# Performance work log

Hardware: AMD Instinct MI355X
Metric: run time of the kernel (lower is better)

Reference implementation:

```python
import jax, jax.numpy as jnp
import numpy as np

NEG_SLOPE = 0.2

def gat_conv(x, src, dst, W, a_src, a_dst, bias, N):
    # PyG GATConv, heads=1: h = xW; e_ij = LeakyReLU(a_src.h_j + a_dst.h_i)
    h = x @ W                                   # [N, H]
    as_ = h @ a_src                             # [N]
    ad_ = h @ a_dst                             # [N]
    e = jax.nn.leaky_relu(as_[src] + ad_[dst], NEG_SLOPE)   # [E]
    m = jax.ops.segment_max(e, dst, num_segments=N)          # per-target max
    w = jnp.exp(e - m[dst])
    denom = jax.ops.segment_sum(w, dst, num_segments=N)
    alpha = w / (denom[dst] + 1e-16)                          # [E]
    out = jax.ops.segment_sum(alpha[:, None] * h[src], dst, num_segments=N)
    return out + bias


def setup_inputs() -> dict:
    key = jax.random.key(0)
    N, E, D, H, A = 20000, 320000, 256, 256, 8
    ks = jax.random.split(key, 16)
    s = lambda k, shp, fan: jax.random.normal(k, shp, jnp.float32) * (1.0 / np.sqrt(fan))
    return {
        "obs": jax.random.normal(ks[0], (N, D), jnp.float32),
        "edge_index": jax.random.randint(ks[1], (2, E), 0, N, dtype=jnp.int32),
        "W1": s(ks[2], (D, H), D), "a1_src": s(ks[3], (H,), H), "a1_dst": s(ks[4], (H,), H), "b1": jnp.zeros((H,), jnp.float32),
        "W2": s(ks[5], (H, H), H), "a2_src": s(ks[6], (H,), H), "a2_dst": s(ks[7], (H,), H), "b2": jnp.zeros((H,), jnp.float32),
        "Wm1": s(ks[8], (H, H), H), "bm1": jnp.zeros((H,), jnp.float32),
        "Wm2": s(ks[9], (H, A), H), "bm2": jnp.zeros((A,), jnp.float32),
    }


def reference(obs, edge_index, W1, a1_src, a1_dst, b1, W2, a2_src, a2_dst, b2, Wm1, bm1, Wm2, bm2):
    N = obs.shape[0]
    loops = jnp.arange(N, dtype=edge_index.dtype)
    src = jnp.concatenate([edge_index[0], loops])   # add self-loops (PyG default)
    dst = jnp.concatenate([edge_index[1], loops])
    x = jax.nn.relu(gat_conv(obs, src, dst, W1, a1_src, a1_dst, b1, N))
    x = jax.nn.relu(gat_conv(x,   src, dst, W2, a2_src, a2_dst, b2, N))
    x = jax.nn.relu(x @ Wm1 + bm1)
    return jnp.tanh(x @ Wm2 + bm2)
```

## Files before the change

### kernel.cpp

```cpp
#include <hip/hip_runtime.h>
#include <hip/hip_bf16.h>
#include <math.h>
#include <stdio.h>

typedef __attribute__((ext_vector_type(8))) short short8;
typedef __attribute__((ext_vector_type(4))) float f32x4;
typedef __attribute__((ext_vector_type(4))) unsigned short us4;
typedef unsigned short ushort_t;

__device__ __forceinline__ float us2f(unsigned short u) {
    return __uint_as_float(((unsigned)u) << 16);
}
__device__ __forceinline__ unsigned short f2us_rtn(float f) {
    return (unsigned short)__bfloat16_as_ushort(__float2bfloat16(f));
}

__global__ void prep3_wT(const float* __restrict__ Wa, const float* __restrict__ Wb,
                         const float* __restrict__ Wc,
                         unsigned short* __restrict__ HiA, unsigned short* __restrict__ LoA,
                         unsigned short* __restrict__ HiB, unsigned short* __restrict__ LoB,
                         unsigned short* __restrict__ HiC, unsigned short* __restrict__ LoC,
                         int K, int Nn) {
    const int tot = K * Nn;
    int idx = blockIdx.x * blockDim.x + threadIdx.x;
    if (idx >= 3 * tot) return;
    const float* W;
    unsigned short *Hi, *Lo;
    if (idx < tot) { W = Wa; Hi = HiA; Lo = LoA; }
    else if (idx < 2 * tot) { W = Wb; Hi = HiB; Lo = LoB; idx -= tot; }
    else { W = Wc; Hi = HiC; Lo = LoC; idx -= 2 * tot; }
    const int n = idx / K, k = idx - n * K;
    const float f = W[(size_t)k * Nn + n];
    const unsigned u = __float_as_uint(f);
    Hi[idx] = (unsigned short)(u >> 16);
    const float hf = __uint_as_float(u & 0xffff0000u);
    Lo[idx] = (unsigned short)(__float_as_uint(f - hf) >> 16);
}

#define LP 40
template <bool BIASRELU>
__global__ __launch_bounds__(256) void gemm_mfma(const float* __restrict__ A,
                                                 const unsigned short* __restrict__ BtHi,
                                                 const unsigned short* __restrict__ BtLo,
                                                 const float* __restrict__ bias,
                                                 unsigned short* __restrict__ C,
                                                 int M, int Nn, int K) {
    __shared__ unsigned short sAhi[64 * LP], sAlo[64 * LP];
    __shared__ unsigned short sBhi[128 * LP], sBlo[128 * LP];
    const int tid = threadIdx.x;
    const int wave = tid >> 6, lane = tid & 63;
    const int m16 = lane & 15, quad = lane >> 4;
    const int row0 = blockIdx.x * 64, col0 = blockIdx.y * 128;
    const int arow = tid >> 3;
    const int akv = (tid & 7) * 4;
    const int bn = tid >> 1;
    const int bk = (tid & 1) * 16;
    const int wr = (wave >> 1) * 32, wc = (wave & 1) * 64;

    f32x4 acc[2][4] = {};
    for (int k0 = 0; k0 < K; k0 += 32) {
#pragma unroll
        for (int i = 0; i < 2; i++) {
            const int r = arow + 32 * i;
            const int grow = row0 + r;
            const int gr = grow < M ? grow : M - 1;
            const float4 a4 = *(const float4*)(A + (size_t)gr * K + k0 + akv);
            const float f[4] = {a4.x, a4.y, a4.z, a4.w};
            us4 hi, lo;
#pragma unroll
            for (int e = 0; e < 4; e++) {
                const unsigned u = __float_as_uint(f[e]);
                hi[e] = (unsigned short)(u >> 16);
                const float hf = __uint_as_float(u & 0xffff0000u);
                lo[e] = (unsigned short)(__float_as_uint(f[e] - hf) >> 16);
            }
            *(us4*)&sAhi[r * LP + akv] = hi;
            *(us4*)&sAlo[r * LP + akv] = lo;
        }
        {
            const size_t gb = (size_t)(col0 + bn) * K + k0 + bk;
            *(short8*)&sBhi[bn * LP + bk]     = *(const short8*)(BtHi + gb);
            *(short8*)&sBhi[bn * LP + bk + 8] = *(const short8*)(BtHi + gb + 8);
            *(short8*)&sBlo[bn * LP + bk]     = *(const short8*)(BtLo + gb);
            *(short8*)&sBlo[bn * LP + bk + 8] = *(const short8*)(BtLo + gb + 8);
        }
        __syncthreads();
        short8 bh[4], bl[4];
#pragma unroll
        for (int ni = 0; ni < 4; ni++) {
            const int nb = (wc + ni * 16 + m16) * LP + quad * 8;
            bh[ni] = *(const short8*)&sBhi[nb];
            bl[ni] = *(const short8*)&sBlo[nb];
        }
#pragma unroll
        for (int mi = 0; mi < 2; mi++) {
            const int ab = (wr + mi * 16 + m16) * LP + quad * 8;
            const short8 ah = *(const short8*)&sAhi[ab];
            const short8 al = *(const short8*)&sAlo[ab];
#pragma unroll
            for (int ni = 0; ni < 4; ni++) {
                acc[mi][ni] = __builtin_amdgcn_mfma_f32_16x16x32_bf16(ah, bh[ni], acc[mi][ni], 0, 0, 0);
                acc[mi][ni] = __builtin_amdgcn_mfma_f32_16x16x32_bf16(ah, bl[ni], acc[mi][ni], 0, 0, 0);
                acc[mi][ni] = __builtin_amdgcn_mfma_f32_16x16x32_bf16(al, bh[ni], acc[mi][ni], 0, 0, 0);
            }
        }
        __syncthreads();
    }
#pragma unroll
    for (int mi = 0; mi < 2; mi++) {
        const int orow_base = row0 + wr + mi * 16 + quad * 4;
#pragma unroll
        for (int ni = 0; ni < 4; ni++) {
            const int ocol = col0 + wc + ni * 16 + m16;
#pragma unroll
            for (int r = 0; r < 4; r++) {
                const int orow = orow_base + r;
                if (orow < M) {
                    float v = acc[mi][ni][r];
                    if (BIASRELU) { v += bias[ocol]; v = fmaxf(v, 0.f); }
                    C[(size_t)orow * Nn + ocol] = f2us_rtn(v);
                }
            }
        }
    }
}
#undef LP

__global__ __launch_bounds__(256) void dots_kernel(const unsigned short* __restrict__ hb,
                                                   const float* __restrict__ asrc,
                                                   const float* __restrict__ adst,
                                                   float* __restrict__ as_,
                                                   float* __restrict__ ad_, int N) {
    const int wave = threadIdx.x >> 6, lane = threadIdx.x & 63;
    const int n = blockIdx.x * 4 + wave;
    if (n >= N) return;
    const int f = lane * 4;
    const us4 v = *(const us4*)(hb + (size_t)n * 256 + f);
    float s1 = 0.f, s2 = 0.f;
#pragma unroll
    for (int e = 0; e < 4; e++) {
        const float x = us2f(v[e]);
        s1 = fmaf(x, asrc[f + e], s1);
        s2 = fmaf(x, adst[f + e], s2);
    }
#pragma unroll
    for (int off = 32; off; off >>= 1) {
        s1 += __shfl_down(s1, off);
        s2 += __shfl_down(s2, off);
    }
    if (lane == 0) { as_[n] = s1; ad_[n] = s2; }
}

__global__ void init_deg(int* __restrict__ deg, int N) {
    const int i = blockIdx.x * blockDim.x + threadIdx.x;
    if (i < N) deg[i] = 0;
}

__global__ void count_kernel(const int* __restrict__ dstA, int* __restrict__ deg, int E, int Etot) {
    const int e = blockIdx.x * blockDim.x + threadIdx.x;
    if (e >= Etot) return;
    const int d = (e < E) ? dstA[e] : (e - E);
    atomicAdd(&deg[d], 1);
}

__global__ __launch_bounds__(1024) void scan_kernel(const int* __restrict__ deg,
                                                    int* __restrict__ offs,
                                                    int* __restrict__ cursor, int N) {
    __shared__ int sums[1024];
    const int t = threadIdx.x;
    const int chunk = (N + 1023) / 1024;
    const int start = t * chunk;
    int s = 0;
    for (int i = 0; i < chunk; i++) {
        const int p = start + i;
        if (p < N) s += deg[p];
    }
    sums[t] = s;
    __syncthreads();
    for (int off = 1; off < 1024; off <<= 1) {
        const int add = (t >= off) ? sums[t - off] : 0;
        __syncthreads();
        sums[t] += add;
        __syncthreads();
    }
    int run = (t > 0) ? sums[t - 1] : 0;
    for (int i = 0; i < chunk; i++) {
        const int p = start + i;
        if (p < N) { offs[p] = run; cursor[p] = run; run += deg[p]; }
    }
    if (t == 0) offs[N] = sums[1023];
}

__global__ void scatter_kernel(const int* __restrict__ srcA, const int* __restrict__ dstA,
                               int* __restrict__ cursor, int* __restrict__ esrc, int E, int Etot) {
    const int e = blockIdx.x * blockDim.x + threadIdx.x;
    if (e >= Etot) return;
    int s, d;
    if (e < E) { s = srcA[e]; d = dstA[e]; } else { s = d = e - E; }
    const int slot = atomicAdd(&cursor[d], 1);
    esrc[slot] = s;
}

__global__ __launch_bounds__(128) void agg_kernel(const unsigned short* __restrict__ hb,
                                                  const int* __restrict__ offs,
                                                  const int* __restrict__ esrc,
                                                  const float* __restrict__ as_,
                                                  const float* __restrict__ ad_,
                                                  const float* __restrict__ bias,
                                                  float* __restrict__ xout, int N) {
    const int n = blockIdx.x;
    const int f0 = threadIdx.x * 2;
    const int b = offs[n], e2 = offs[n + 1];
    const float adn = ad_[n];
    float ax = 0.f, ay = 0.f, wsum = 0.f;
    int j = b;
    for (; j + 8 <= e2; j += 8) {
        int s[8];
#pragma unroll
        for (int u = 0; u < 8; u++) s[u] = esrc[j + u];
        unsigned pv[8];
#pragma unroll
        for (int u = 0; u < 8; u++) pv[u] = *(const unsigned*)(hb + (size_t)s[u] * 256 + f0);
        float w[8];
#pragma unroll
        for (int u = 0; u < 8; u++) {
            float v = as_[s[u]] + adn;
            v = v > 0.f ? v : 0.2f * v;
            w[u] = __expf(v);
        }
#pragma unroll
        for (int u = 0; u < 8; u++) {
            ax = fmaf(w[u], us2f((unsigned short)(pv[u] & 0xffffu)), ax);
            ay = fmaf(w[u], us2f((unsigned short)(pv[u] >> 16)), ay);
            wsum += w[u];
        }
    }
    for (; j < e2; j++) {
        const int s = esrc[j];
        float v = as_[s] + adn;
        v = v > 0.f ? v : 0.2f * v;
        const float w = __expf(v);
        const unsigned pv = *(const unsigned*)(hb + (size_t)s * 256 + f0);
        ax = fmaf(w, us2f((unsigned short)(pv & 0xffffu)), ax);
        ay = fmaf(w, us2f((unsigned short)(pv >> 16)), ay);
        wsum += w;
    }
    const float inv = 1.0f / (wsum + 1e-16f);
    const float rx = ax * inv + bias[f0];
    const float ry = ay * inv + bias[f0 + 1];
    xout[(size_t)n * 256 + f0]     = rx > 0.f ? rx : 0.f;
    xout[(size_t)n * 256 + f0 + 1] = ry > 0.f ? ry : 0.f;
}

__global__ __launch_bounds__(256) void final_kernel(const unsigned short* __restrict__ xb,
                                                    const float* __restrict__ W,
                                                    const float* __restrict__ bias,
                                                    float* __restrict__ out, int N, int A) {
    const int wave = threadIdx.x >> 6, lane = threadIdx.x & 63;
    const int n = blockIdx.x * 4 + wave;
    if (n >= N) return;
    const int k0 = lane * 4;
    const us4 v = *(const us4*)(xb + (size_t)n * 256 + k0);
    float p[8] = {};
#pragma unroll
    for (int e = 0; e < 4; e++) {
        const float xv = us2f(v[e]);
#pragma unroll
        for (int a = 0; a < 8; a++) p[a] = fmaf(xv, W[(k0 + e) * A + a], p[a]);
    }
#pragma unroll
    for (int off = 32; off; off >>= 1)
#pragma unroll
        for (int a = 0; a < 8; a++) p[a] += __shfl_down(p[a], off);
    if (lane == 0) {
        for (int a = 0; a < A; a++) out[(size_t)n * A + a] = tanhf(p[a] + bias[a]);
    }
}

__device__ __forceinline__ float wdot64(const float* a, const float* b, int K, int bstride) {
    const int lane = threadIdx.x & 63;
    float s = 0.f;
    for (int k = lane; k < K; k += 64) s = fmaf(a[k], b[(size_t)k * bstride], s);
#pragma unroll
    for (int off = 32; off; off >>= 1) s += __shfl_down(s, off);
    return __shfl(s, 0);
}
__global__ void probe_gemm(const float* X, const float* W, const unsigned short* hb,
                           int K, int Nn) {
    const float h00 = wdot64(X, W, K, Nn);
    const float h05 = wdot64(X, W + 5, K, Nn);
    if ((threadIdx.x & 63) != 0) return;
    const float g0 = us2f(hb[0]), g5 = us2f(hb[5]);
    const bool bad0 = fabsf(h00 - g0) > 1.5e-2f + 1e-2f * fabsf(h00);
    const bool bad5 = fabsf(h05 - g5) > 1.5e-2f + 1e-2f * fabsf(h05);
    if (bad0 || bad5)
        printf("BADMFMA ref=(%e,%e) got=(%e,%e)\n", (double)h00, (double)h05,
               (double)g0, (double)g5);
}
__global__ void guard_kernel(const float* __restrict__ out) {
    if (threadIdx.x != 0 || blockIdx.x != 0) return;
    const float o0 = out[0];
    if (fabsf(o0) > 0.f && o0 == o0) return;
    printf("GUARD o0=%e o1=%e\n", (double)o0, (double)out[1]);
}

extern "C" void kernel_launch(void* const* d_in, const int* in_sizes, int n_in,
                              void* d_out, int out_size, void* d_ws, size_t ws_size,
                              hipStream_t stream) {
    const float* obs = (const float*)d_in[0];
    const int* eidx  = (const int*)d_in[1];
    const float* W1  = (const float*)d_in[2];
    const float* a1s = (const float*)d_in[3];
    const float* a1d = (const float*)d_in[4];
    const float* b1  = (const float*)d_in[5];
    const float* W2  = (const float*)d_in[6];
    const float* a2s = (const float*)d_in[7];
    const float* a2d = (const float*)d_in[8];
    const float* b2v = (const float*)d_in[9];
    const float* Wm1 = (const float*)d_in[10];
    const float* bm1 = (const float*)d_in[11];
    const float* Wm2 = (const float*)d_in[12];
    const float* bm2 = (const float*)d_in[13];
    float* out = (float*)d_out;

    const int Hh = in_sizes[3];
    const int Dd = in_sizes[2] / Hh;
    const int N  = in_sizes[0] / Dd;
    const int E  = in_sizes[1] / 2;
    const int Etot = E + N;
    const int Aout = in_sizes[12] / Hh;

    const int* srcA = eidx;
    const int* dstA = eidx + E;

    size_t off = 0;
    char* ws = (char*)d_ws;
    auto alloc = [&](size_t bytes) -> char* {
        char* p = ws + off;
        off = (off + bytes + 15) & ~(size_t)15;
        return p;
    };
    unsigned short* h = (unsigned short*)alloc((size_t)N * Hh * 2);
    float* xbuf  = (float*)alloc((size_t)N * Hh * 4);
    float* as_   = (float*)alloc((size_t)N * 4);
    float* ad_   = (float*)alloc((size_t)N * 4);
    int* deg     = (int*)alloc((size_t)N * 4);
    int* offs    = (int*)alloc((size_t)(N + 1) * 4);
    int* cursor  = (int*)alloc((size_t)N * 4);
    int* esrc    = (int*)alloc((size_t)Etot * 4);
    const size_t wsz = (size_t)Dd * Hh;
    unsigned short* W1tH = (unsigned short*)alloc(wsz * 2);
    unsigned short* W1tL = (unsigned short*)alloc(wsz * 2);
    unsigned short* W2tH = (unsigned short*)alloc(wsz * 2);
    unsigned short* W2tL = (unsigned short*)alloc(wsz * 2);
    unsigned short* WmtH = (unsigned short*)alloc(wsz * 2);
    unsigned short* WmtL = (unsigned short*)alloc(wsz * 2);

    const int eb = 256;
    const int eg = (Etot + eb - 1) / eb;
    const int ng = (N + 255) / 256;
    const dim3 ggrid((N + 63) / 64, Hh / 128);
    const int nb4 = (N + 3) / 4;

    const int p3 = (3 * (int)wsz + 255) / 256;
    prep3_wT<<<p3, 256, 0, stream>>>(W1, W2, Wm1, W1tH, W1tL, W2tH, W2tL, WmtH, WmtL, Dd, Hh);

    init_deg<<<ng, 256, 0, stream>>>(deg, N);
    count_kernel<<<eg, eb, 0, stream>>>(dstA, deg, E, Etot);
    scan_kernel<<<1, 1024, 0, stream>>>(deg, offs, cursor, N);
    scatter_kernel<<<eg, eb, 0, stream>>>(srcA, dstA, cursor, esrc, E, Etot);

    gemm_mfma<false><<<ggrid, 256, 0, stream>>>(obs, W1tH, W1tL, nullptr, h, N, Hh, Dd);
    probe_gemm<<<1, 64, 0, stream>>>(obs, W1, h, Dd, Hh);
    dots_kernel<<<nb4, 256, 0, stream>>>(h, a1s, a1d, as_, ad_, N);
    agg_kernel<<<N, 128, 0, stream>>>(h, offs, esrc, as_, ad_, b1, xbuf, N);

    gemm_mfma<false><<<ggrid, 256, 0, stream>>>(xbuf, W2tH, W2tL, nullptr, h, N, Hh, Hh);
    dots_kernel<<<nb4, 256, 0, stream>>>(h, a2s, a2d, as_, ad_, N);
    agg_kernel<<<N, 128, 0, stream>>>(h, offs, esrc, as_, ad_, b2v, xbuf, N);

    gemm_mfma<true><<<ggrid, 256, 0, stream>>>(xbuf, WmtH, WmtL, bm1, h, N, Hh, Hh);
    final_kernel<<<nb4, 256, 0, stream>>>(h, Wm2, bm2, out, N, Aout);

    guard_kernel<<<1, 64, 0, stream>>>(out);
}
```

Baseline: 310.7 us.

## Store GEMM activations as bf16 and drop the A-lo split term

Activations are now bf16 everywhere. The obs input is converted once by a new prep kernel, and the aggregation kernel writes bf16 output instead of fp32. The GEMM loads bf16 A tiles directly and keeps only the two hi/lo products on B, so the third MFMA per step goes away. The K tile grows from 32 to 64 and the debug probe kernel is removed. This halves activation traffic and cuts MFMA work, but activation precision drops to plain bf16 and the larger tile uses more LDS.

```diff
diff --git a/kernel.cpp b/kernel.cpp
--- a/kernel.cpp
+++ b/kernel.cpp
@@ -6,7 +6,7 @@
 typedef __attribute__((ext_vector_type(8))) short short8;
 typedef __attribute__((ext_vector_type(4))) float f32x4;
 typedef __attribute__((ext_vector_type(4))) unsigned short us4;
-typedef unsigned short ushort_t;
+typedef unsigned short us_t;
 
 __device__ __forceinline__ float us2f(unsigned short u) {
     return __uint_as_float(((unsigned)u) << 16);
@@ -37,71 +37,70 @@
     Lo[idx] = (unsigned short)(__float_as_uint(f - hf) >> 16);
 }
 
-#define LP 40
+__global__ void prep_obs(const float* __restrict__ X, unsigned short* __restrict__ Xb, int tot8) {
+    const int i = blockIdx.x * blockDim.x + threadIdx.x;
+    if (i >= tot8) return;
+    const float4 a = *(const float4*)(X + (size_t)i * 8);
+    const float4 b = *(const float4*)(X + (size_t)i * 8 + 4);
+    short8 o;
+    const float f[8] = {a.x, a.y, a.z, a.w, b.x, b.y, b.z, b.w};
+#pragma unroll
+    for (int e = 0; e < 8; e++) o[e] = (short)f2us_rtn(f[e]);
+    *(short8*)(Xb + (size_t)i * 8) = o;
+}
+
+#define LP 72
 template <bool BIASRELU>
-__global__ __launch_bounds__(256) void gemm_mfma(const float* __restrict__ A,
+__global__ __launch_bounds__(256) void gemm_mfma(const unsigned short* __restrict__ A,
                                                  const unsigned short* __restrict__ BtHi,
                                                  const unsigned short* __restrict__ BtLo,
                                                  const float* __restrict__ bias,
                                                  unsigned short* __restrict__ C,
                                                  int M, int Nn, int K) {
-    __shared__ unsigned short sAhi[64 * LP], sAlo[64 * LP];
-    __shared__ unsigned short sBhi[128 * LP], sBlo[128 * LP];
+    __shared__ unsigned short sA[64 * LP];
+    __shared__ unsigned short sBh[128 * LP];
+    __shared__ unsigned short sBl[128 * LP];
     const int tid = threadIdx.x;
     const int wave = tid >> 6, lane = tid & 63;
     const int m16 = lane & 15, quad = lane >> 4;
     const int row0 = blockIdx.x * 64, col0 = blockIdx.y * 128;
-    const int arow = tid >> 3;
-    const int akv = (tid & 7) * 4;
-    const int bn = tid >> 1;
-    const int bk = (tid & 1) * 16;
     const int wr = (wave >> 1) * 32, wc = (wave & 1) * 64;
+    const int ar = tid >> 2, akc = (tid & 3) * 8;
+    const int bkc = (tid & 7) * 8, bcb = tid >> 3;
 
     f32x4 acc[2][4] = {};
-    for (int k0 = 0; k0 < K; k0 += 32) {
-#pragma unroll
-        for (int i = 0; i < 2; i++) {
-            const int r = arow + 32 * i;
-            const int grow = row0 + r;
-            const int gr = grow < M ? grow : M - 1;
-            const float4 a4 = *(const float4*)(A + (size_t)gr * K + k0 + akv);
-            const float f[4] = {a4.x, a4.y, a4.z, a4.w};
-            us4 hi, lo;
-#pragma unroll
-            for (int e = 0; e < 4; e++) {
-                const unsigned u = __float_as_uint(f[e]);
-                hi[e] = (unsigned short)(u >> 16);
-                const float hf = __uint_as_float(u & 0xffff0000u);
-                lo[e] = (unsigned short)(__float_as_uint(f[e] - hf) >> 16);
-            }
-            *(us4*)&sAhi[r * LP + akv] = hi;
-            *(us4*)&sAlo[r * LP + akv] = lo;
-        }
+    for (int k0 = 0; k0 < K; k0 += 64) {
         {
-            const size_t gb = (size_t)(col0 + bn) * K + k0 + bk;
-            *(short8*)&sBhi[bn * LP + bk]     = *(const short8*)(BtHi + gb);
-            *(short8*)&sBhi[bn * LP + bk + 8] = *(const short8*)(BtHi + gb + 8);
-            *(short8*)&sBlo[bn * LP + bk]     = *(const short8*)(BtLo + gb);
-            *(short8*)&sBlo[bn * LP + bk + 8] = *(const short8*)(BtLo + gb + 8);
+            const int gr = (row0 + ar) < M ? (row0 + ar) : (M - 1);
+            const unsigned short* Ap = A + (size_t)gr * K + k0 + akc;
+            *(short8*)&sA[ar * LP + akc]      = *(const short8*)Ap;
+            *(short8*)&sA[ar * LP + akc + 32] = *(const short8*)(Ap + 32);
+        }
+#pragma unroll
+        for (int q = 0; q < 8; q++) {
+            const int pl = q >> 2;
+            const int colq = bcb + 32 * (q & 3);
+            const unsigned short* Bp = (pl ? BtLo : BtHi) + (size_t)(col0 + colq) * K + k0 + bkc;
+            unsigned short* sB = pl ? sBl : sBh;
+            *(short8*)&sB[colq * LP + bkc] = *(const short8*)Bp;
         }
         __syncthreads();
-        short8 bh[4], bl[4];
-#pragma unroll
-        for (int ni = 0; ni < 4; ni++) {
-            const int nb = (wc + ni * 16 + m16) * LP + quad * 8;
-            bh[ni] = *(const short8*)&sBhi[nb];
-            bl[ni] = *(const short8*)&sBlo[nb];
-        }
-#pragma unroll
-        for (int mi = 0; mi < 2; mi++) {
-            const int ab = (wr + mi * 16 + m16) * LP + quad * 8;
-            const short8 ah = *(const short8*)&sAhi[ab];
-            const short8 al = *(const short8*)&sAlo[ab];
+#pragma unroll
+        for (int ks = 0; ks < 2; ks++) {
+            short8 ah[2];
+#pragma unroll
+            for (int mi = 0; mi < 2; mi++)
+                ah[mi] = *(const short8*)&sA[(wr + mi * 16 + m16) * LP + ks * 32 + quad * 8];
 #pragma unroll
             for (int ni = 0; ni < 4; ni++) {
-                acc[mi][ni] = __builtin_amdgcn_mfma_f32_16x16x32_bf16(ah, bh[ni], acc[mi][ni], 0, 0, 0);
-                acc[mi][ni] = __builtin_amdgcn_mfma_f32_16x16x32_bf16(ah, bl[ni], acc[mi][ni], 0, 0, 0);
-                acc[mi][ni] = __builtin_amdgcn_mfma_f32_16x16x32_bf16(al, bh[ni], acc[mi][ni], 0, 0, 0);
+                const int nb = (wc + ni * 16 + m16) * LP + ks * 32 + quad * 8;
+                const short8 bh = *(const short8*)&sBh[nb];
+                const short8 bl = *(const short8*)&sBl[nb];
+#pragma unroll
+                for (int mi = 0; mi < 2; mi++) {
+                    acc[mi][ni] = __builtin_amdgcn_mfma_f32_16x16x32_bf16(ah[mi], bh, acc[mi][ni], 0, 0, 0);
+                    acc[mi][ni] = __builtin_amdgcn_mfma_f32_16x16x32_bf16(ah[mi], bl, acc[mi][ni], 0, 0, 0);
+                }
             }
         }
         __syncthreads();
@@ -207,7 +206,7 @@
                                                   const float* __restrict__ as_,
                                                   const float* __restrict__ ad_,
                                                   const float* __restrict__ bias,
-                                                  float* __restrict__ xout, int N) {
+                                                  unsigned short* __restrict__ xout, int N) {
     const int n = blockIdx.x;
     const int f0 = threadIdx.x * 2;
     const int b = offs[n], e2 = offs[n + 1];
@@ -246,10 +245,12 @@
         wsum += w;
     }
     const float inv = 1.0f / (wsum + 1e-16f);
-    const float rx = ax * inv + bias[f0];
-    const float ry = ay * inv + bias[f0 + 1];
-    xout[(size_t)n * 256 + f0]     = rx > 0.f ? rx : 0.f;
-    xout[(size_t)n * 256 + f0 + 1] = ry > 0.f ? ry : 0.f;
+    float rx = ax * inv + bias[f0];
+    float ry = ay * inv + bias[f0 + 1];
+    rx = rx > 0.f ? rx : 0.f;
+    ry = ry > 0.f ? ry : 0.f;
+    const unsigned pack = (unsigned)f2us_rtn(rx) | ((unsigned)f2us_rtn(ry) << 16);
+    *(unsigned*)(xout + (size_t)n * 256 + f0) = pack;
 }
 
 __global__ __launch_bounds__(256) void final_kernel(const unsigned short* __restrict__ xb,
@@ -277,26 +278,6 @@
     }
 }
 
-__device__ __forceinline__ float wdot64(const float* a, const float* b, int K, int bstride) {
-    const int lane = threadIdx.x & 63;
-    float s = 0.f;
-    for (int k = lane; k < K; k += 64) s = fmaf(a[k], b[(size_t)k * bstride], s);
-#pragma unroll
-    for (int off = 32; off; off >>= 1) s += __shfl_down(s, off);
-    return __shfl(s, 0);
-}
-__global__ void probe_gemm(const float* X, const float* W, const unsigned short* hb,
-                           int K, int Nn) {
-    const float h00 = wdot64(X, W, K, Nn);
-    const float h05 = wdot64(X, W + 5, K, Nn);
-    if ((threadIdx.x & 63) != 0) return;
-    const float g0 = us2f(hb[0]), g5 = us2f(hb[5]);
-    const bool bad0 = fabsf(h00 - g0) > 1.5e-2f + 1e-2f * fabsf(h00);
-    const bool bad5 = fabsf(h05 - g5) > 1.5e-2f + 1e-2f * fabsf(h05);
-    if (bad0 || bad5)
-        printf("BADMFMA ref=(%e,%e) got=(%e,%e)\n", (double)h00, (double)h05,
-               (double)g0, (double)g5);
-}
 __global__ void guard_kernel(const float* __restrict__ out) {
     if (threadIdx.x != 0 || blockIdx.x != 0) return;
     const float o0 = out[0];
@@ -340,8 +321,9 @@
         off = (off + bytes + 15) & ~(size_t)15;
         return p;
     };
-    unsigned short* h = (unsigned short*)alloc((size_t)N * Hh * 2);
-    float* xbuf  = (float*)alloc((size_t)N * Hh * 4);
+    unsigned short* obs_b = (unsigned short*)alloc((size_t)N * Dd * 2);
+    unsigned short* h     = (unsigned short*)alloc((size_t)N * Hh * 2);
+    unsigned short* xb    = (unsigned short*)alloc((size_t)N * Hh * 2);
     float* as_   = (float*)alloc((size_t)N * 4);
     float* ad_   = (float*)alloc((size_t)N * 4);
     int* deg     = (int*)alloc((size_t)N * 4);
@@ -364,22 +346,23 @@
 
     const int p3 = (3 * (int)wsz + 255) / 256;
     prep3_wT<<<p3, 256, 0, stream>>>(W1, W2, Wm1, W1tH, W1tL, W2tH, W2tL, WmtH, WmtL, Dd, Hh);
+    const int tot8 = (N * Dd) / 8;
+    prep_obs<<<(tot8 + 255) / 256, 256, 0, stream>>>(obs, obs_b, tot8);
 
     init_deg<<<ng, 256, 0, stream>>>(deg, N);
     count_kernel<<<eg, eb, 0, stream>>>(dstA, deg, E, Etot);
     scan_kernel<<<1, 1024, 0, stream>>>(deg, offs, cursor, N);
     scatter_kernel<<<eg, eb, 0, stream>>>(srcA, dstA, cursor, esrc, E, Etot);
 
-    gemm_mfma<false><<<ggrid, 256, 0, stream>>>(obs, W1tH, W1tL, nullptr, h, N, Hh, Dd);
-    probe_gemm<<<1, 64, 0, stream>>>(obs, W1, h, Dd, Hh);
+    gemm_mfma<false><<<ggrid, 256, 0, stream>>>(obs_b, W1tH, W1tL, nullptr, h, N, Hh, Dd);
     dots_kernel<<<nb4, 256, 0, stream>>>(h, a1s, a1d, as_, ad_, N);
-    agg_kernel<<<N, 128, 0, stream>>>(h, offs, esrc, as_, ad_, b1, xbuf, N);
-
-    gemm_mfma<false><<<ggrid, 256, 0, stream>>>(xbuf, W2tH, W2tL, nullptr, h, N, Hh, Hh);
+    agg_kernel<<<N, 128, 0, stream>>>(h, offs, esrc, as_, ad_, b1, xb, N);
+
+    gemm_mfma<false><<<ggrid, 256, 0, stream>>>(xb, W2tH, W2tL, nullptr, h, N, Hh, Hh);
     dots_kernel<<<nb4, 256, 0, stream>>>(h, a2s, a2d, as_, ad_, N);
-    agg_kernel<<<N, 128, 0, stream>>>(h, offs, esrc, as_, ad_, b2v, xbuf, N);
-
-    gemm_mfma<true><<<ggrid, 256, 0, stream>>>(xbuf, WmtH, WmtL, bm1, h, N, Hh, Hh);
+    agg_kernel<<<N, 128, 0, stream>>>(h, offs, esrc, as_, ad_, b2v, xb, N);
+
+    gemm_mfma<true><<<ggrid, 256, 0, stream>>>(xb, WmtH, WmtL, bm1, h, N, Hh, Hh);
     final_kernel<<<nb4, 256, 0, stream>>>(h, Wm2, bm2, out, N, Aout);
 
     guard_kernel<<<1, 64, 0, stream>>>(out);
```

New measurement: 302.7 us. 2.6% less time.
